# Kernel tuning notes

Hardware: AMD Instinct MI355X
Metric: run time of the kernel (lower is better)

## Reference

```python
import jax, jax.numpy as jnp
import numpy as np

CH = 16        # channel_n
HID = 128      # hidden_size
IN_CH = 3      # input_channels (locked each step)
FIRE_RATE = 0.5


def _dwconv3x3(x, w, b):
    # depthwise 3x3, reflect padding (torch padding_mode='reflect', padding=1)
    xp = jnp.pad(x, ((0, 0), (0, 0), (1, 1), (1, 1)), mode='reflect')
    y = jax.lax.conv_general_dilated(
        xp, w, window_strides=(1, 1), padding='VALID',
        dimension_numbers=('NCHW', 'OIHW', 'NCHW'), feature_group_count=CH)
    return y + b[None, :, None, None]


def _conv1x1(x, w, b=None):
    # w: (out_ch, in_ch) -- squeezed 1x1 conv kernel
    y = jnp.einsum('bchw,oc->bohw', x, w)
    return y if b is None else y + b[None, :, None, None]


def setup_inputs() -> dict:
    key = jax.random.key(0)
    ks = jax.random.split(key, 8)
    B, H, W = 4, 256, 256
    x = jax.random.normal(ks[0], (B, CH, H, W), dtype=jnp.float32)
    # depthwise kernels: (CH, 1, 3, 3)
    p0_w = jax.random.normal(ks[1], (CH, 1, 3, 3), dtype=jnp.float32) * (1.0 / 3.0)
    p0_b = jax.random.normal(ks[2], (CH,), dtype=jnp.float32) * 0.1
    p1_w = jax.random.normal(ks[3], (CH, 1, 3, 3), dtype=jnp.float32) * (1.0 / 3.0)
    p1_b = jax.random.normal(ks[4], (CH,), dtype=jnp.float32) * 0.1
    # fc0: Conv2d(3*CH -> HID, k=1); fc1: Conv2d(HID -> CH, k=1, bias=False)
    fc0_w = jax.random.normal(ks[5], (HID, 3 * CH), dtype=jnp.float32) * (1.0 / np.sqrt(3 * CH))
    fc0_b = jax.random.normal(ks[6], (HID,), dtype=jnp.float32) * 0.1
    # NOTE: torch zero-inits fc1; we use small random weights so the reference is non-trivial.
    fc1_w = jax.random.normal(ks[7], (CH, HID), dtype=jnp.float32) * (0.1 / np.sqrt(HID))
    return {"x": x, "p0_w": p0_w, "p0_b": p0_b, "p1_w": p1_w, "p1_b": p1_b,
            "fc0_w": fc0_w, "fc0_b": fc0_b, "fc1_w": fc1_w, "steps": 32}


def reference(x, p0_w, p0_b, p1_w, p1_b, fc0_w, fc0_b, fc1_w, steps):
    B, _, H, W = x.shape
    input_image = x[:, :IN_CH]  # clone of input channels, re-written each step
    keys = jax.random.split(jax.random.key(42), steps)

    @jax.checkpoint
    def step(x, key):
        # perceive: depthwise 3x3 x2, concat with state
        z1 = _dwconv3x3(x, p0_w, p0_b)
        z2 = _dwconv3x3(x, p1_w, p1_b)
        y = jnp.concatenate([x, z1, z2], axis=1)        # [B, 3*CH, H, W]
        # 1x1-conv MLP
        dx = jax.nn.relu(_conv1x1(y, fc0_w, fc0_b))      # [B, HID, H, W]
        dx = _conv1x1(dx, fc1_w)                         # [B, CH, H, W]
        # stochastic fire mask: rand > fire_rate, broadcast over channels
        mask = (jax.random.uniform(key, (B, 1, H, W), dtype=x.dtype) > FIRE_RATE).astype(x.dtype)
        x = x + dx * mask                                # residual update
        x = x.at[:, :IN_CH].set(input_image)             # channel lock
        return x, None

    x, _ = jax.lax.scan(step, x, keys)
    out = x[:, 3]  # segmentation channel
    return out, x
```

## Files before the change

### kernel.cpp

```cpp
#include <hip/hip_runtime.h>
#include <cstdint>

#define CH     16
#define HPIX   256
#define WPIX   256
#define BATCH  4
#define HID    128
#define STEPS  32
#define PLANE  (HPIX * WPIX)
#define MASK_N (BATCH * PLANE)

#define TW 16
#define TH 8
#define XTW 18
#define XTH 10
#define NPX (XTH * XTW)
#define HSF 20

typedef _Float16 half8  __attribute__((ext_vector_type(8)));
typedef _Float16 half4e __attribute__((ext_vector_type(4)));
typedef float floatx4  __attribute__((ext_vector_type(4)));
typedef float floatx16 __attribute__((ext_vector_type(16)));

__host__ __device__ static inline void tf2x32(uint32_t k0, uint32_t k1,
                                              uint32_t x0, uint32_t x1,
                                              uint32_t& o0, uint32_t& o1) {
  const uint32_t ks2 = k0 ^ k1 ^ 0x1BD11BDAu;
#define TFROT(a) { x0 += x1; x1 = (x1 << (a)) | (x1 >> (32 - (a))); x1 ^= x0; }
  x0 += k0;  x1 += k1;
  TFROT(13) TFROT(15) TFROT(26) TFROT(6)
  x0 += k1;  x1 += ks2 + 1u;
  TFROT(17) TFROT(29) TFROT(16) TFROT(24)
  x0 += ks2; x1 += k0 + 2u;
  TFROT(13) TFROT(15) TFROT(26) TFROT(6)
  x0 += k0;  x1 += k1 + 3u;
  TFROT(17) TFROT(29) TFROT(16) TFROT(24)
  x0 += k1;  x1 += ks2 + 4u;
  TFROT(13) TFROT(15) TFROT(26) TFROT(6)
  x0 += ks2; x1 += k0 + 5u;
#undef TFROT
  o0 = x0; o1 = x1;
}

__global__ __launch_bounds__(256) void prep_weights(
    const float* __restrict__ fc0_w, const float* __restrict__ fc0_b,
    const float* __restrict__ fc1_w,
    const float* __restrict__ p0_w, const float* __restrict__ p0_b,
    const float* __restrict__ p1_w, const float* __restrict__ p1_b,
    _Float16* __restrict__ Mh, _Float16* __restrict__ W1h,
    float* __restrict__ bp) {
  const int idx = blockIdx.x * 256 + threadIdx.x;
  if (idx < 9 * HID * CH) {
    const int tap = idx / (HID * CH);
    const int rem = idx - tap * (HID * CH);
    const int h = rem >> 4, c = rem & 15;
    float m = fc0_w[h * 48 + 16 + c] * p0_w[c * 9 + tap]
            + fc0_w[h * 48 + 32 + c] * p1_w[c * 9 + tap];
    if (tap == 4) m += fc0_w[h * 48 + c];
    Mh[(tap * HID + h) * CH + c] = (_Float16)m;
  } else if (idx < 9 * HID * CH + CH * HID) {
    const int i2 = idx - 9 * HID * CH;
    W1h[i2] = (_Float16)fc1_w[i2];
  } else if (idx < 9 * HID * CH + CH * HID + HID) {
    const int h = idx - (9 * HID * CH + CH * HID);
    float s = fc0_b[h];
    for (int c = 0; c < CH; ++c)
      s += fc0_w[h * 48 + 16 + c] * p0_b[c]
         + fc0_w[h * 48 + 32 + c] * p1_b[c];
    bp[h] = s;
  }
}

__global__ __launch_bounds__(256) void nca_step(
    const float* __restrict__ x_in, float* __restrict__ x_out,
    const float* __restrict__ x0,
    const _Float16* __restrict__ Mh, const _Float16* __restrict__ W1h,
    const float* __restrict__ bp,
    uint32_t k0, uint32_t k1, int wrgb) {
  __shared__ __align__(16) _Float16 halo[NPX * HSF];
  __shared__ __align__(16) _Float16 Hbuf[64 * HID];
  __shared__ float maskbuf[128];

  const int tid = threadIdx.x;
  const int w0 = blockIdx.x * TW;
  const int h0 = blockIdx.y * TH;
  const int b  = blockIdx.z;

  const int wv   = tid >> 6;
  const int lane = tid & 63;
  const int n    = lane & 15;
  const int g    = lane >> 4;
  const int c32  = lane & 31;
  const int q2   = lane >> 5;

  const float* __restrict__ xb  = x_in + (size_t)b * CH * PLANE;
  const float* __restrict__ x0b = x0   + (size_t)b * CH * PLANE;

  half8 Atap[9];
  #pragma unroll
  for (int t = 0; t < 9; ++t)
    Atap[t] = *(const half8*)(Mh + ((t * HID + 32 * wv + c32) << 4) + 8 * q2);
  half8 bw1[4];
  #pragma unroll
  for (int s = 0; s < 4; ++s)
    bw1[s] = *(const half8*)(W1h + n * HID + 32 * s + 8 * g);
  float4 bias4[4];
  #pragma unroll
  for (int rb = 0; rb < 4; ++rb)
    bias4[rb] = *(const float4*)(bp + 32 * wv + 8 * rb + 4 * q2);

  float4 xcv[2];
  size_t xoff[2];
  #pragma unroll
  for (int i = 0; i < 2; ++i) {
    xoff[i] = (size_t)n * PLANE + (size_t)(h0 + 4 * i + wv) * WPIX + w0 + 4 * g;
    xcv[i] = *(const float4*)(((n < 3) ? x0b : xb) + xoff[i]);
  }

  if (tid < NPX) {
    const int hr = tid / XTW, hc = tid - (tid / XTW) * XTW;
    int gh = h0 + hr - 1;
    gh = (gh < 0) ? -gh : ((gh > HPIX - 1) ? (2 * (HPIX - 1) - gh) : gh);
    int gw = w0 + hc - 1;
    gw = (gw < 0) ? -gw : ((gw > WPIX - 1) ? (2 * (WPIX - 1) - gw) : gw);
    const float* __restrict__ srcS = xb  + gh * WPIX + gw;
    const float* __restrict__ src0 = x0b + gh * WPIX + gw;
    #pragma unroll
    for (int blk = 0; blk < 4; ++blk) {
      half4e h4;
      #pragma unroll
      for (int e = 0; e < 4; ++e) {
        const int c = 4 * blk + e;
        h4[e] = (_Float16)((c < 3 ? src0 : srcS)[(size_t)c * PLANE]);
      }
      *(half4e*)(halo + tid * HSF + 4 * blk) = h4;
    }
  }

  if (lane < 32) {
    const int pxl = wv * 32 + lane;
    const int hp = h0 + (pxl >> 4), wp = w0 + (pxl & 15);
    const uint32_t j = (uint32_t)(b * PLANE + hp * WPIX + wp);
    uint32_t r0, r1;
    tf2x32(k0, k1, 0u, j, r0, r1);
    const uint32_t bits = r0 ^ r1;
    union { uint32_t i; float f; } cvt;
    cvt.i = (bits >> 9) | 0x3F800000u;
    maskbuf[pxl] = ((cvt.f - 1.0f) > 0.5f) ? 1.0f : 0.0f;
  }
  __syncthreads();

  float* __restrict__ xob = x_out + (size_t)b * CH * PLANE;

  #pragma unroll
  for (int half = 0; half < 2; ++half) {
    #pragma unroll
    for (int cti = 0; cti < 2; ++cti) {
      const int ct   = 2 * half + cti;
      const int prow = 2 * ct + (c32 >> 4);
      const int pcol = c32 & 15;
      half8 btap[9];
      #pragma unroll
      for (int dr = 0; dr < 3; ++dr) {
        #pragma unroll
        for (int dj = 0; dj < 3; ++dj) {
          const _Float16* hp =
              halo + ((prow + dr) * XTW + pcol + dj) * HSF + 8 * q2;
          const half4e lo = *(const half4e*)hp;
          const half4e hi = *(const half4e*)(hp + 4);
          half8 ff;
          ff[0] = lo[0]; ff[1] = lo[1]; ff[2] = lo[2]; ff[3] = lo[3];
          ff[4] = hi[0]; ff[5] = hi[1]; ff[6] = hi[2]; ff[7] = hi[3];
          btap[dr * 3 + dj] = ff;
        }
      }
      floatx16 acc = {0.f,0.f,0.f,0.f,0.f,0.f,0.f,0.f,
                      0.f,0.f,0.f,0.f,0.f,0.f,0.f,0.f};
      #pragma unroll
      for (int t = 0; t < 9; ++t)
        acc = __builtin_amdgcn_mfma_f32_32x32x16_f16(Atap[t], btap[t], acc,
                                                     0, 0, 0);
      const int px  = 32 * ct + c32;
      const int ph  = px & 63;
      const int n16 = px & 15;
      #pragma unroll
      for (int rb = 0; rb < 4; ++rb) {
        half4e hv;
        hv[0] = (_Float16)fmaxf(acc[4 * rb + 0] + bias4[rb].x, 0.f);
        hv[1] = (_Float16)fmaxf(acc[4 * rb + 1] + bias4[rb].y, 0.f);
        hv[2] = (_Float16)fmaxf(acc[4 * rb + 2] + bias4[rb].z, 0.f);
        hv[3] = (_Float16)fmaxf(acc[4 * rb + 3] + bias4[rb].w, 0.f);
        *(half4e*)(Hbuf + ph * HID + (((4 * wv + rb) ^ n16) << 3) + 4 * q2) = hv;
      }
    }
    __syncthreads();

    {
      const int ct2 = 4 * half + wv;
      floatx4 c2 = {0.f, 0.f, 0.f, 0.f};
      #pragma unroll
      for (int ks = 0; ks < 4; ++ks) {
        const half8 a2 = *(const half8*)(
            Hbuf + (16 * (ct2 & 3) + n) * HID + (((4 * ks + g) ^ n) << 3));
        c2 = __builtin_amdgcn_mfma_f32_16x16x32_f16(a2, bw1[ks], c2, 0, 0, 0);
      }
      const float4 mk = *(const float4*)(maskbuf + 16 * ct2 + 4 * g);
      const float4 xc = xcv[half];
      float4 res;
      res.x = (n < 3) ? xc.x : fmaf(mk.x, c2[0], xc.x);
      res.y = (n < 3) ? xc.y : fmaf(mk.y, c2[1], xc.y);
      res.z = (n < 3) ? xc.z : fmaf(mk.z, c2[2], xc.z);
      res.w = (n < 3) ? xc.w : fmaf(mk.w, c2[3], xc.w);
      if (n >= 3 || wrgb)
        *(float4*)(xob + xoff[half]) = res;
    }
    if (half == 0) __syncthreads();
  }
}

__global__ __launch_bounds__(256) void extract_ch3(
    const float* __restrict__ xf, float* __restrict__ out) {
  const int i = blockIdx.x * 256 + threadIdx.x;
  if (i >= MASK_N) return;
  const int b = i >> 16;
  const int p = i & (PLANE - 1);
  out[i] = xf[((size_t)b * CH + 3) * PLANE + p];
}

extern "C" void kernel_launch(void* const* d_in, const int* in_sizes, int n_in,
                              void* d_out, int out_size, void* d_ws, size_t ws_size,
                              hipStream_t stream) {
  const float* x     = (const float*)d_in[0];
  const float* p0_w  = (const float*)d_in[1];
  const float* p0_b  = (const float*)d_in[2];
  const float* p1_w  = (const float*)d_in[3];
  const float* p1_b  = (const float*)d_in[4];
  const float* fc0_w = (const float*)d_in[5];
  const float* fc0_b = (const float*)d_in[6];
  const float* fc1_w = (const float*)d_in[7];

  uint32_t kk[STEPS][2];
  for (int i = 0; i < STEPS; ++i) {
    uint32_t a, b2;
    tf2x32(0u, 42u, 0u, (uint32_t)i, a, b2);
    kk[i][0] = a;
    kk[i][1] = b2;
  }

  float* out = (float*)d_out;
  _Float16* Mh  = (_Float16*)d_out;
  _Float16* W1h = Mh + 9 * HID * CH;
  float*    bpr = (float*)((char*)d_out + (9 * HID * CH + CH * HID) * 2);
  float* bufA = out + MASK_N;
  float* bufB = (float*)d_ws;

  const int prep_n = 9 * HID * CH + CH * HID + HID;
  prep_weights<<<dim3((prep_n + 255) / 256), dim3(256), 0, stream>>>(
      fc0_w, fc0_b, fc1_w, p0_w, p0_b, p1_w, p1_b, Mh, W1h, bpr);

  const dim3 grid(WPIX / TW, HPIX / TH, BATCH);
  const dim3 block(256);

  for (int i = 0; i < STEPS; ++i) {
    const float* src = (i == 0) ? x : ((i & 1) ? bufB : bufA);
    float* dst = (i & 1) ? bufA : bufB;
    nca_step<<<grid, block, 0, stream>>>(src, dst, x, Mh, W1h, bpr,
                                         kk[i][0], kk[i][1],
                                         (i == STEPS - 1) ? 1 : 0);
  }
  extract_ch3<<<dim3(MASK_N / 256), dim3(256), 0, stream>>>(bufA, out);
}
```

Before: 692.2 us.

## Add fp16 pixel-interleaved shadow state and precompute fire-mask bitmaps

Keeps a second copy of the state in fp16 with the 16 channels of each pixel stored together, so the halo load becomes two 16-byte reads per pixel instead of 16 strided fp32 loads. Each step also writes this shadow copy for the next step. The per-step Threefry fire-mask generation moves into a single upfront kernel that packs all step masks into bitmaps, and nca_step reads those bits. The cost is extra global writes for the shadow and scattered 2-byte stores, plus two setup kernels. Channels 0-2 of shB are seeded once, and since the shadow is never written for them later, the locked channels stay valid.

```diff
diff --git a/kernel.cpp b/kernel.cpp
--- a/kernel.cpp
+++ b/kernel.cpp
@@ -21,6 +21,8 @@
 typedef _Float16 half4e __attribute__((ext_vector_type(4)));
 typedef float floatx4  __attribute__((ext_vector_type(4)));
 typedef float floatx16 __attribute__((ext_vector_type(16)));
+
+struct KeyBlob { uint32_t k[2 * STEPS]; };
 
 __host__ __device__ static inline void tf2x32(uint32_t k0, uint32_t k1,
                                               uint32_t x0, uint32_t x1,
@@ -71,15 +73,48 @@
   }
 }
 
+__global__ __launch_bounds__(256) void init_shadow(
+    const float* __restrict__ x,
+    _Float16* __restrict__ shA, _Float16* __restrict__ shB) {
+  const int i = blockIdx.x * 256 + threadIdx.x;
+  const int b = i >> 16;
+  const int p = i & (PLANE - 1);
+  const float* __restrict__ xp = x + (size_t)b * CH * PLANE + p;
+  half8 lo, hi;
+  #pragma unroll
+  for (int c = 0; c < 8; ++c) lo[c] = (_Float16)xp[(size_t)c * PLANE];
+  #pragma unroll
+  for (int c = 0; c < 8; ++c) hi[c] = (_Float16)xp[(size_t)(c + 8) * PLANE];
+  _Float16* d = shA + (size_t)i * CH;
+  *(half8*)(d)     = lo;
+  *(half8*)(d + 8) = hi;
+  _Float16* d2 = shB + (size_t)i * CH;
+  d2[0] = lo[0]; d2[1] = lo[1]; d2[2] = lo[2];
+}
+
+__global__ __launch_bounds__(256) void prep_masks(
+    KeyBlob ks, uint64_t* __restrict__ mb) {
+  const uint32_t t = blockIdx.x * 256 + threadIdx.x;
+  const uint32_t step = t >> 18;
+  const uint32_t j = t & (MASK_N - 1);
+  uint32_t r0, r1;
+  tf2x32(ks.k[2 * step], ks.k[2 * step + 1], 0u, j, r0, r1);
+  const uint32_t bits = r0 ^ r1;
+  union { uint32_t i; float f; } cvt;
+  cvt.i = (bits >> 9) | 0x3F800000u;
+  const unsigned long long ball = __ballot((cvt.f - 1.0f) > 0.5f);
+  if ((threadIdx.x & 63) == 0) mb[t >> 6] = ball;
+}
+
 __global__ __launch_bounds__(256) void nca_step(
     const float* __restrict__ x_in, float* __restrict__ x_out,
     const float* __restrict__ x0,
+    const _Float16* __restrict__ sh_src, _Float16* __restrict__ sh_dst,
     const _Float16* __restrict__ Mh, const _Float16* __restrict__ W1h,
-    const float* __restrict__ bp,
-    uint32_t k0, uint32_t k1, int wrgb) {
+    const float* __restrict__ bp, const uint32_t* __restrict__ mb,
+    int wrgb) {
   __shared__ __align__(16) _Float16 halo[NPX * HSF];
   __shared__ __align__(16) _Float16 Hbuf[64 * HID];
-  __shared__ float maskbuf[128];
 
   const int tid = threadIdx.x;
   const int w0 = blockIdx.x * TW;
@@ -123,30 +158,13 @@
     gh = (gh < 0) ? -gh : ((gh > HPIX - 1) ? (2 * (HPIX - 1) - gh) : gh);
     int gw = w0 + hc - 1;
     gw = (gw < 0) ? -gw : ((gw > WPIX - 1) ? (2 * (WPIX - 1) - gw) : gw);
-    const float* __restrict__ srcS = xb  + gh * WPIX + gw;
-    const float* __restrict__ src0 = x0b + gh * WPIX + gw;
-    #pragma unroll
-    for (int blk = 0; blk < 4; ++blk) {
-      half4e h4;
-      #pragma unroll
-      for (int e = 0; e < 4; ++e) {
-        const int c = 4 * blk + e;
-        h4[e] = (_Float16)((c < 3 ? src0 : srcS)[(size_t)c * PLANE]);
-      }
-      *(half4e*)(halo + tid * HSF + 4 * blk) = h4;
-    }
-  }
-
-  if (lane < 32) {
-    const int pxl = wv * 32 + lane;
-    const int hp = h0 + (pxl >> 4), wp = w0 + (pxl & 15);
-    const uint32_t j = (uint32_t)(b * PLANE + hp * WPIX + wp);
-    uint32_t r0, r1;
-    tf2x32(k0, k1, 0u, j, r0, r1);
-    const uint32_t bits = r0 ^ r1;
-    union { uint32_t i; float f; } cvt;
-    cvt.i = (bits >> 9) | 0x3F800000u;
-    maskbuf[pxl] = ((cvt.f - 1.0f) > 0.5f) ? 1.0f : 0.0f;
+    const uint4* __restrict__ sp = (const uint4*)(
+        sh_src + ((size_t)b * PLANE + (size_t)gh * WPIX + gw) * CH);
+    const uint4 va = sp[0];
+    const uint4 vb = sp[1];
+    uint32_t* hd = (uint32_t*)(halo + tid * HSF);
+    hd[0] = va.x; hd[1] = va.y; hd[2] = va.z; hd[3] = va.w;
+    hd[4] = vb.x; hd[5] = vb.y; hd[6] = vb.z; hd[7] = vb.w;
   }
   __syncthreads();
 
@@ -204,15 +222,28 @@
             Hbuf + (16 * (ct2 & 3) + n) * HID + (((4 * ks + g) ^ n) << 3));
         c2 = __builtin_amdgcn_mfma_f32_16x16x32_f16(a2, bw1[ks], c2, 0, 0, 0);
       }
-      const float4 mk = *(const float4*)(maskbuf + 16 * ct2 + 4 * g);
+      const uint32_t j = (uint32_t)b * PLANE
+                       + (uint32_t)(h0 + 4 * half + wv) * WPIX
+                       + (uint32_t)(w0 + 4 * g);
+      const uint32_t mw = mb[j >> 5];
+      const uint32_t sh = j & 31u;
       const float4 xc = xcv[half];
       float4 res;
-      res.x = (n < 3) ? xc.x : fmaf(mk.x, c2[0], xc.x);
-      res.y = (n < 3) ? xc.y : fmaf(mk.y, c2[1], xc.y);
-      res.z = (n < 3) ? xc.z : fmaf(mk.z, c2[2], xc.z);
-      res.w = (n < 3) ? xc.w : fmaf(mk.w, c2[3], xc.w);
+      res.x = (n < 3) ? xc.x : (((mw >> (sh + 0)) & 1u) ? xc.x + c2[0] : xc.x);
+      res.y = (n < 3) ? xc.y : (((mw >> (sh + 1)) & 1u) ? xc.y + c2[1] : xc.y);
+      res.z = (n < 3) ? xc.z : (((mw >> (sh + 2)) & 1u) ? xc.z + c2[2] : xc.z);
+      res.w = (n < 3) ? xc.w : (((mw >> (sh + 3)) & 1u) ? xc.w + c2[3] : xc.w);
       if (n >= 3 || wrgb)
         *(float4*)(xob + xoff[half]) = res;
+      if (n >= 3) {
+        _Float16* dp = sh_dst
+            + ((size_t)b * PLANE + (size_t)(h0 + 4 * half + wv) * WPIX
+               + (w0 + 4 * g)) * CH + n;
+        dp[0]  = (_Float16)res.x;
+        dp[16] = (_Float16)res.y;
+        dp[32] = (_Float16)res.z;
+        dp[48] = (_Float16)res.w;
+      }
     }
     if (half == 0) __syncthreads();
   }
@@ -239,12 +270,12 @@
   const float* fc0_b = (const float*)d_in[6];
   const float* fc1_w = (const float*)d_in[7];
 
-  uint32_t kk[STEPS][2];
+  KeyBlob hk;
   for (int i = 0; i < STEPS; ++i) {
     uint32_t a, b2;
     tf2x32(0u, 42u, 0u, (uint32_t)i, a, b2);
-    kk[i][0] = a;
-    kk[i][1] = b2;
+    hk.k[2 * i]     = a;
+    hk.k[2 * i + 1] = b2;
   }
 
   float* out = (float*)d_out;
@@ -254,9 +285,16 @@
   float* bufA = out + MASK_N;
   float* bufB = (float*)d_ws;
 
+  _Float16* shA   = (_Float16*)((char*)d_ws + ((size_t)32 << 20));
+  _Float16* shB   = (_Float16*)((char*)d_ws + ((size_t)48 << 20));
+  uint32_t* mbits = (uint32_t*)((char*)d_ws + ((size_t)64 << 20));
+
   const int prep_n = 9 * HID * CH + CH * HID + HID;
   prep_weights<<<dim3((prep_n + 255) / 256), dim3(256), 0, stream>>>(
       fc0_w, fc0_b, fc1_w, p0_w, p0_b, p1_w, p1_b, Mh, W1h, bpr);
+  init_shadow<<<dim3(MASK_N / 256), dim3(256), 0, stream>>>(x, shA, shB);
+  prep_masks<<<dim3((STEPS * MASK_N) / 256), dim3(256), 0, stream>>>(
+      hk, (uint64_t*)mbits);
 
   const dim3 grid(WPIX / TW, HPIX / TH, BATCH);
   const dim3 block(256);
@@ -264,8 +302,11 @@
   for (int i = 0; i < STEPS; ++i) {
     const float* src = (i == 0) ? x : ((i & 1) ? bufB : bufA);
     float* dst = (i & 1) ? bufA : bufB;
-    nca_step<<<grid, block, 0, stream>>>(src, dst, x, Mh, W1h, bpr,
-                                         kk[i][0], kk[i][1],
+    const _Float16* ssrc = (i & 1) ? shB : shA;
+    _Float16*       sdst = (i & 1) ? shA : shB;
+    nca_step<<<grid, block, 0, stream>>>(src, dst, x, ssrc, sdst,
+                                         Mh, W1h, bpr,
+                                         mbits + (size_t)i * (MASK_N / 32),
                                          (i == STEPS - 1) ? 1 : 0);
   }
   extract_ch3<<<dim3(MASK_N / 256), dim3(256), 0, stream>>>(bufA, out);
```

Result: slower. 785.2 us (+13.4%).

## Widen tile to 32x8 and fuse channel-3 extraction into last step

Applied to the files above, without the earlier changes.

Doubles the spatial tile width from 16 to 32 pixels so each block processes 256 pixels in four passes. This cuts the halo overhead per pixel and halves the grid size. The separate extract_ch3 kernel is removed; the final step writes channel 3 directly to the output, and the weight scratch moves from the output buffer into the workspace. The change adds more serial passes and syncs per block, raises shared memory for the halo, and reduces the number of blocks, which may lower occupancy.

```diff
diff --git a/kernel.cpp b/kernel.cpp
--- a/kernel.cpp
+++ b/kernel.cpp
@@ -10,9 +10,9 @@
 #define PLANE  (HPIX * WPIX)
 #define MASK_N (BATCH * PLANE)
 
-#define TW 16
+#define TW 32
 #define TH 8
-#define XTW 18
+#define XTW 34
 #define XTH 10
 #define NPX (XTH * XTW)
 #define HSF 20
@@ -76,10 +76,10 @@
     const float* __restrict__ x0,
     const _Float16* __restrict__ Mh, const _Float16* __restrict__ W1h,
     const float* __restrict__ bp,
-    uint32_t k0, uint32_t k1, int wrgb) {
+    uint32_t k0, uint32_t k1, int wrgb, float* __restrict__ outp) {
   __shared__ __align__(16) _Float16 halo[NPX * HSF];
   __shared__ __align__(16) _Float16 Hbuf[64 * HID];
-  __shared__ float maskbuf[128];
+  __shared__ float maskbuf[TW * TH];
 
   const int tid = threadIdx.x;
   const int w0 = blockIdx.x * TW;
@@ -109,16 +109,18 @@
   for (int rb = 0; rb < 4; ++rb)
     bias4[rb] = *(const float4*)(bp + 32 * wv + 8 * rb + 4 * q2);
 
-  float4 xcv[2];
-  size_t xoff[2];
-  #pragma unroll
-  for (int i = 0; i < 2; ++i) {
-    xoff[i] = (size_t)n * PLANE + (size_t)(h0 + 4 * i + wv) * WPIX + w0 + 4 * g;
-    xcv[i] = *(const float4*)(((n < 3) ? x0b : xb) + xoff[i]);
-  }
-
-  if (tid < NPX) {
-    const int hr = tid / XTW, hc = tid - (tid / XTW) * XTW;
+  float4 xcv[4];
+  size_t xoff[4];
+  #pragma unroll
+  for (int k = 0; k < 4; ++k) {
+    xoff[k] = (size_t)n * PLANE
+            + (size_t)(h0 + 2 * k + (wv >> 1)) * WPIX
+            + w0 + 16 * (wv & 1) + 4 * g;
+    xcv[k] = *(const float4*)(((n < 3) ? x0b : xb) + xoff[k]);
+  }
+
+  for (int t = tid; t < NPX; t += 256) {
+    const int hr = t / XTW, hc = t - (t / XTW) * XTW;
     int gh = h0 + hr - 1;
     gh = (gh < 0) ? -gh : ((gh > HPIX - 1) ? (2 * (HPIX - 1) - gh) : gh);
     int gw = w0 + hc - 1;
@@ -133,39 +135,36 @@
         const int c = 4 * blk + e;
         h4[e] = (_Float16)((c < 3 ? src0 : srcS)[(size_t)c * PLANE]);
       }
-      *(half4e*)(halo + tid * HSF + 4 * blk) = h4;
+      *(half4e*)(halo + t * HSF + 4 * blk) = h4;
     }
   }
 
-  if (lane < 32) {
-    const int pxl = wv * 32 + lane;
-    const int hp = h0 + (pxl >> 4), wp = w0 + (pxl & 15);
+  {
+    const int hp = h0 + (tid >> 5), wp = w0 + (tid & 31);
     const uint32_t j = (uint32_t)(b * PLANE + hp * WPIX + wp);
     uint32_t r0, r1;
     tf2x32(k0, k1, 0u, j, r0, r1);
     const uint32_t bits = r0 ^ r1;
     union { uint32_t i; float f; } cvt;
     cvt.i = (bits >> 9) | 0x3F800000u;
-    maskbuf[pxl] = ((cvt.f - 1.0f) > 0.5f) ? 1.0f : 0.0f;
+    maskbuf[tid] = ((cvt.f - 1.0f) > 0.5f) ? 1.0f : 0.0f;
   }
   __syncthreads();
 
   float* __restrict__ xob = x_out + (size_t)b * CH * PLANE;
 
   #pragma unroll
-  for (int half = 0; half < 2; ++half) {
+  for (int k = 0; k < 4; ++k) {
     #pragma unroll
     for (int cti = 0; cti < 2; ++cti) {
-      const int ct   = 2 * half + cti;
-      const int prow = 2 * ct + (c32 >> 4);
-      const int pcol = c32 & 15;
+      const int ct = 2 * k + cti;
       half8 btap[9];
       #pragma unroll
       for (int dr = 0; dr < 3; ++dr) {
         #pragma unroll
         for (int dj = 0; dj < 3; ++dj) {
           const _Float16* hp =
-              halo + ((prow + dr) * XTW + pcol + dj) * HSF + 8 * q2;
+              halo + ((ct + dr) * XTW + c32 + dj) * HSF + 8 * q2;
           const half4e lo = *(const half4e*)hp;
           const half4e hi = *(const half4e*)(hp + 4);
           half8 ff;
@@ -180,9 +179,8 @@
       for (int t = 0; t < 9; ++t)
         acc = __builtin_amdgcn_mfma_f32_32x32x16_f16(Atap[t], btap[t], acc,
                                                      0, 0, 0);
-      const int px  = 32 * ct + c32;
-      const int ph  = px & 63;
-      const int n16 = px & 15;
+      const int ph  = 32 * cti + c32;
+      const int n16 = c32 & 15;
       #pragma unroll
       for (int rb = 0; rb < 4; ++rb) {
         half4e hv;
@@ -196,35 +194,31 @@
     __syncthreads();
 
     {
-      const int ct2 = 4 * half + wv;
       floatx4 c2 = {0.f, 0.f, 0.f, 0.f};
       #pragma unroll
       for (int ks = 0; ks < 4; ++ks) {
         const half8 a2 = *(const half8*)(
-            Hbuf + (16 * (ct2 & 3) + n) * HID + (((4 * ks + g) ^ n) << 3));
+            Hbuf + (16 * wv + n) * HID + (((4 * ks + g) ^ n) << 3));
         c2 = __builtin_amdgcn_mfma_f32_16x16x32_f16(a2, bw1[ks], c2, 0, 0, 0);
       }
-      const float4 mk = *(const float4*)(maskbuf + 16 * ct2 + 4 * g);
-      const float4 xc = xcv[half];
+      const int prow = 2 * k + (wv >> 1);
+      const int pcol = 16 * (wv & 1) + 4 * g;
+      const float4 mk = *(const float4*)(maskbuf + prow * TW + pcol);
+      const float4 xc = xcv[k];
       float4 res;
       res.x = (n < 3) ? xc.x : fmaf(mk.x, c2[0], xc.x);
       res.y = (n < 3) ? xc.y : fmaf(mk.y, c2[1], xc.y);
       res.z = (n < 3) ? xc.z : fmaf(mk.z, c2[2], xc.z);
       res.w = (n < 3) ? xc.w : fmaf(mk.w, c2[3], xc.w);
       if (n >= 3 || wrgb)
-        *(float4*)(xob + xoff[half]) = res;
+        *(float4*)(xob + xoff[k]) = res;
+      if (wrgb && n == 3) {
+        *(float4*)(outp + (size_t)b * PLANE
+                   + (size_t)(h0 + prow) * WPIX + w0 + pcol) = res;
+      }
     }
-    if (half == 0) __syncthreads();
-  }
-}
-
-__global__ __launch_bounds__(256) void extract_ch3(
-    const float* __restrict__ xf, float* __restrict__ out) {
-  const int i = blockIdx.x * 256 + threadIdx.x;
-  if (i >= MASK_N) return;
-  const int b = i >> 16;
-  const int p = i & (PLANE - 1);
-  out[i] = xf[((size_t)b * CH + 3) * PLANE + p];
+    if (k < 3) __syncthreads();
+  }
 }
 
 extern "C" void kernel_launch(void* const* d_in, const int* in_sizes, int n_in,
@@ -248,11 +242,12 @@
   }
 
   float* out = (float*)d_out;
-  _Float16* Mh  = (_Float16*)d_out;
-  _Float16* W1h = Mh + 9 * HID * CH;
-  float*    bpr = (float*)((char*)d_out + (9 * HID * CH + CH * HID) * 2);
   float* bufA = out + MASK_N;
   float* bufB = (float*)d_ws;
+
+  _Float16* Mh  = (_Float16*)((char*)d_ws + ((size_t)32 << 20));
+  _Float16* W1h = Mh + 9 * HID * CH;
+  float*    bpr = (float*)((char*)W1h + CH * HID * 2);
 
   const int prep_n = 9 * HID * CH + CH * HID + HID;
   prep_weights<<<dim3((prep_n + 255) / 256), dim3(256), 0, stream>>>(
@@ -266,7 +261,6 @@
     float* dst = (i & 1) ? bufA : bufB;
     nca_step<<<grid, block, 0, stream>>>(src, dst, x, Mh, W1h, bpr,
                                          kk[i][0], kk[i][1],
-                                         (i == STEPS - 1) ? 1 : 0);
-  }
-  extract_ch3<<<dim3(MASK_N / 256), dim3(256), 0, stream>>>(bufA, out);
-}
+                                         (i == STEPS - 1) ? 1 : 0, out);
+  }
+}
```

Measured after the change: 759.4 us. 1.1x slower.

## Carry NCA state as fp16 channel-last buffers and fuse final output write

Applied to the files above, without the earlier changes.

The state passed between steps becomes an fp16 array with 16 channels contiguous per pixel, built once by a new init kernel. Each halo pixel is then loaded with two 16-byte reads instead of sixteen strided fp32 plane reads. The residual base is read from the fp16 halo in shared memory rather than re-read in fp32 from global memory. The last step writes the fp32 final state and channel 3 directly, which removes the separate extract kernel. The cost is that the residual state is now rounded to fp16 on every one of the 32 steps, which may add error against the fp32 reference.

```diff
diff --git a/kernel.cpp b/kernel.cpp
--- a/kernel.cpp
+++ b/kernel.cpp
@@ -40,6 +40,10 @@
   x0 += ks2; x1 += k0 + 5u;
 #undef TFROT
   o0 = x0; o1 = x1;
+}
+
+__device__ __forceinline__ int refl(int v) {
+  return v < 0 ? -v : (v > HPIX - 1 ? 2 * (HPIX - 1) - v : v);
 }
 
 __global__ __launch_bounds__(256) void prep_weights(
@@ -71,12 +75,29 @@
   }
 }
 
+__global__ __launch_bounds__(256) void init_state(
+    const float* __restrict__ x, _Float16* __restrict__ S) {
+  const int i = blockIdx.x * 256 + threadIdx.x;
+  const int b = i >> 16;
+  const int p = i & (PLANE - 1);
+  const float* __restrict__ xp = x + (size_t)b * CH * PLANE + p;
+  half8 lo, hi;
+  #pragma unroll
+  for (int c = 0; c < 8; ++c) lo[c] = (_Float16)xp[(size_t)c * PLANE];
+  #pragma unroll
+  for (int c = 0; c < 8; ++c) hi[c] = (_Float16)xp[(size_t)(c + 8) * PLANE];
+  _Float16* d = S + (size_t)i * CH;
+  *(half8*)(d)     = lo;
+  *(half8*)(d + 8) = hi;
+}
+
 __global__ __launch_bounds__(256) void nca_step(
-    const float* __restrict__ x_in, float* __restrict__ x_out,
+    const _Float16* __restrict__ s_in, _Float16* __restrict__ s_out,
     const float* __restrict__ x0,
     const _Float16* __restrict__ Mh, const _Float16* __restrict__ W1h,
     const float* __restrict__ bp,
-    uint32_t k0, uint32_t k1, int wrgb) {
+    uint32_t k0, uint32_t k1, int wrgb,
+    float* __restrict__ xfinal, float* __restrict__ outp) {
   __shared__ __align__(16) _Float16 halo[NPX * HSF];
   __shared__ __align__(16) _Float16 Hbuf[64 * HID];
   __shared__ float maskbuf[128];
@@ -93,9 +114,6 @@
   const int c32  = lane & 31;
   const int q2   = lane >> 5;
 
-  const float* __restrict__ xb  = x_in + (size_t)b * CH * PLANE;
-  const float* __restrict__ x0b = x0   + (size_t)b * CH * PLANE;
-
   half8 Atap[9];
   #pragma unroll
   for (int t = 0; t < 9; ++t)
@@ -109,48 +127,32 @@
   for (int rb = 0; rb < 4; ++rb)
     bias4[rb] = *(const float4*)(bp + 32 * wv + 8 * rb + 4 * q2);
 
-  float4 xcv[2];
-  size_t xoff[2];
-  #pragma unroll
-  for (int i = 0; i < 2; ++i) {
-    xoff[i] = (size_t)n * PLANE + (size_t)(h0 + 4 * i + wv) * WPIX + w0 + 4 * g;
-    xcv[i] = *(const float4*)(((n < 3) ? x0b : xb) + xoff[i]);
-  }
-
   if (tid < NPX) {
     const int hr = tid / XTW, hc = tid - (tid / XTW) * XTW;
-    int gh = h0 + hr - 1;
-    gh = (gh < 0) ? -gh : ((gh > HPIX - 1) ? (2 * (HPIX - 1) - gh) : gh);
-    int gw = w0 + hc - 1;
-    gw = (gw < 0) ? -gw : ((gw > WPIX - 1) ? (2 * (WPIX - 1) - gw) : gw);
-    const float* __restrict__ srcS = xb  + gh * WPIX + gw;
-    const float* __restrict__ src0 = x0b + gh * WPIX + gw;
-    #pragma unroll
-    for (int blk = 0; blk < 4; ++blk) {
-      half4e h4;
-      #pragma unroll
-      for (int e = 0; e < 4; ++e) {
-        const int c = 4 * blk + e;
-        h4[e] = (_Float16)((c < 3 ? src0 : srcS)[(size_t)c * PLANE]);
-      }
-      *(half4e*)(halo + tid * HSF + 4 * blk) = h4;
-    }
-  }
-
-  if (lane < 32) {
-    const int pxl = wv * 32 + lane;
-    const int hp = h0 + (pxl >> 4), wp = w0 + (pxl & 15);
-    const uint32_t j = (uint32_t)(b * PLANE + hp * WPIX + wp);
+    const int gh = refl(h0 + hr - 1);
+    const int gw = refl(w0 + hc - 1);
+    const uint4* __restrict__ sp = (const uint4*)(
+        s_in + ((size_t)b * PLANE + (size_t)gh * WPIX + gw) * CH);
+    const uint4 va = sp[0];
+    const uint4 vb = sp[1];
+    uint32_t* hd = (uint32_t*)(halo + tid * HSF);
+    hd[0] = va.x; hd[1] = va.y; hd[2] = va.z; hd[3] = va.w;
+    hd[4] = vb.x; hd[5] = vb.y; hd[6] = vb.z; hd[7] = vb.w;
+  }
+
+  if (tid < 128) {
+    const int tr = tid >> 4, tc = tid & 15;
+    const uint32_t j = (uint32_t)(b * PLANE + (h0 + tr) * WPIX + (w0 + tc));
     uint32_t r0, r1;
     tf2x32(k0, k1, 0u, j, r0, r1);
     const uint32_t bits = r0 ^ r1;
     union { uint32_t i; float f; } cvt;
     cvt.i = (bits >> 9) | 0x3F800000u;
-    maskbuf[pxl] = ((cvt.f - 1.0f) > 0.5f) ? 1.0f : 0.0f;
+    maskbuf[tid] = ((cvt.f - 1.0f) > 0.5f) ? 1.0f : 0.0f;
   }
   __syncthreads();
 
-  float* __restrict__ xob = x_out + (size_t)b * CH * PLANE;
+  const float* __restrict__ x0b = x0 + (size_t)b * CH * PLANE;
 
   #pragma unroll
   for (int half = 0; half < 2; ++half) {
@@ -205,26 +207,35 @@
         c2 = __builtin_amdgcn_mfma_f32_16x16x32_f16(a2, bw1[ks], c2, 0, 0, 0);
       }
       const float4 mk = *(const float4*)(maskbuf + 16 * ct2 + 4 * g);
-      const float4 xc = xcv[half];
-      float4 res;
-      res.x = (n < 3) ? xc.x : fmaf(mk.x, c2[0], xc.x);
-      res.y = (n < 3) ? xc.y : fmaf(mk.y, c2[1], xc.y);
-      res.z = (n < 3) ? xc.z : fmaf(mk.z, c2[2], xc.z);
-      res.w = (n < 3) ? xc.w : fmaf(mk.w, c2[3], xc.w);
-      if (n >= 3 || wrgb)
-        *(float4*)(xob + xoff[half]) = res;
+      const float mka[4] = {mk.x, mk.y, mk.z, mk.w};
+      const int hb = ((ct2 + 1) * XTW + 4 * g + 1) * HSF + n;
+      float r[4];
+      #pragma unroll
+      for (int e = 0; e < 4; ++e) {
+        const float bx = (float)halo[hb + e * HSF];
+        r[e] = (n < 3) ? bx : fmaf(mka[e], c2[e], bx);
+      }
+      _Float16* dp = s_out
+          + ((size_t)b * PLANE + (size_t)(h0 + ct2) * WPIX + w0 + 4 * g) * CH
+          + n;
+      dp[0 * CH] = (_Float16)r[0];
+      dp[1 * CH] = (_Float16)r[1];
+      dp[2 * CH] = (_Float16)r[2];
+      dp[3 * CH] = (_Float16)r[3];
+      if (wrgb) {
+        const size_t xoff = (size_t)n * PLANE
+                          + (size_t)(h0 + ct2) * WPIX + w0 + 4 * g;
+        float4 o;
+        if (n < 3) o = *(const float4*)(x0b + xoff);
+        else { o.x = r[0]; o.y = r[1]; o.z = r[2]; o.w = r[3]; }
+        *(float4*)(xfinal + (size_t)b * CH * PLANE + xoff) = o;
+        if (n == 3)
+          *(float4*)(outp + (size_t)b * PLANE
+                     + (size_t)(h0 + ct2) * WPIX + w0 + 4 * g) = o;
+      }
     }
     if (half == 0) __syncthreads();
   }
-}
-
-__global__ __launch_bounds__(256) void extract_ch3(
-    const float* __restrict__ xf, float* __restrict__ out) {
-  const int i = blockIdx.x * 256 + threadIdx.x;
-  if (i >= MASK_N) return;
-  const int b = i >> 16;
-  const int p = i & (PLANE - 1);
-  out[i] = xf[((size_t)b * CH + 3) * PLANE + p];
 }
 
 extern "C" void kernel_launch(void* const* d_in, const int* in_sizes, int n_in,
@@ -247,26 +258,29 @@
     kk[i][1] = b2;
   }
 
-  float* out = (float*)d_out;
-  _Float16* Mh  = (_Float16*)d_out;
+  float* out    = (float*)d_out;
+  float* xfinal = out + MASK_N;
+
+  _Float16* Mh  = (_Float16*)((char*)d_ws + ((size_t)32 << 20));
   _Float16* W1h = Mh + 9 * HID * CH;
-  float*    bpr = (float*)((char*)d_out + (9 * HID * CH + CH * HID) * 2);
-  float* bufA = out + MASK_N;
-  float* bufB = (float*)d_ws;
+  float*    bpr = (float*)((char*)W1h + CH * HID * 2);
+  _Float16* S0  = (_Float16*)((char*)d_ws + ((size_t)40 << 20));
+  _Float16* S1  = (_Float16*)((char*)d_ws + ((size_t)56 << 20));
 
   const int prep_n = 9 * HID * CH + CH * HID + HID;
   prep_weights<<<dim3((prep_n + 255) / 256), dim3(256), 0, stream>>>(
       fc0_w, fc0_b, fc1_w, p0_w, p0_b, p1_w, p1_b, Mh, W1h, bpr);
+  init_state<<<dim3(MASK_N / 256), dim3(256), 0, stream>>>(x, S0);
 
   const dim3 grid(WPIX / TW, HPIX / TH, BATCH);
   const dim3 block(256);
 
   for (int i = 0; i < STEPS; ++i) {
-    const float* src = (i == 0) ? x : ((i & 1) ? bufB : bufA);
-    float* dst = (i & 1) ? bufA : bufB;
+    const _Float16* src = (i & 1) ? S1 : S0;
+    _Float16*       dst = (i & 1) ? S0 : S1;
     nca_step<<<grid, block, 0, stream>>>(src, dst, x, Mh, W1h, bpr,
                                          kk[i][0], kk[i][1],
-                                         (i == STEPS - 1) ? 1 : 0);
-  }
-  extract_ch3<<<dim3(MASK_N / 256), dim3(256), 0, stream>>>(bufA, out);
-}
+                                         (i == STEPS - 1) ? 1 : 0,
+                                         xfinal, out);
+  }
+}
```

Result: no change. 691.6 us (-0.1%).
